# Optimization experiments

Hardware: AMD Instinct MI355X
Metric: run time of the kernel (lower is better)

Reference implementation:

```python
import jax, jax.numpy as jnp
import numpy as np

B, S, QW, HID, HEADS = 1, 4096, 512, 512, 8
D = HID // HEADS  # size_per_head = 64
SCALE = 1.0 / np.sqrt(float(D))


def setup_inputs() -> dict:
    key = jax.random.key(0)
    k1, k2, k3, k4, k5 = jax.random.split(key, 5)
    return {
        "tensor_q": jax.random.normal(k1, (B, S, QW), dtype=jnp.float32),
        "tensor_k": jax.random.normal(k2, (B, S, QW), dtype=jnp.float32),
        "tensor_v": jax.random.normal(k3, (B, S, QW), dtype=jnp.float32),
        # in_proj_layer: [3*hidden, q_width] (torch uses rand uniform init; randn fine for reference)
        "in_proj": jax.random.normal(k4, (3 * HID, QW), dtype=jnp.float32) * 0.02,
        # out_proj: nn.Linear(hidden, out, bias=False) weight shape [out, hidden]
        "w_out": jax.random.normal(k5, (HID, HID), dtype=jnp.float32) * 0.02,
    }


def reference(tensor_q, tensor_k, tensor_v, in_proj, w_out):
    b, s, _ = tensor_q.shape
    wq, wk, wv = in_proj[:HID], in_proj[HID:2 * HID], in_proj[2 * HID:]
    # mm(W, x_2d^T)^T  ==  x_2d @ W^T ; reshape to [b, s, heads, d]
    q = (tensor_q.reshape(-1, QW) @ wq.T).reshape(b, s, HEADS, D)
    k = (tensor_k.reshape(-1, QW) @ wk.T).reshape(b, s, HEADS, D)
    v = (tensor_v.reshape(-1, QW) @ wv.T).reshape(b, s, HEADS, D)
    # scores: [b, h, s_q, s_k], explicitly materialized as in the source
    scores = jnp.einsum('bqhd,bkhd->bhqk', q, k) * SCALE
    probs = jax.nn.softmax(scores, axis=-1)
    ctx = jnp.einsum('bhqk,bkhd->bqhd', probs, v).reshape(b * s, HID)
    out = ctx @ w_out.T
    return out.reshape(b, s, HID)
```

## Files before the change

### kernel.cpp

```cpp
#include <hip/hip_runtime.h>
#include <hip/hip_bf16.h>

#define S_LEN 4096
#define QW_K  512
#define HID_N 512
#define HEADS 8
#define DH    64
#define QSCALE (0.125f * 1.4426950408889634f)

typedef _Float16 f16;
typedef _Float16 half8  __attribute__((ext_vector_type(8)));
typedef _Float16 half4v __attribute__((ext_vector_type(4)));
typedef float    float4v __attribute__((ext_vector_type(4)));
typedef float    f32x16 __attribute__((ext_vector_type(16)));
typedef unsigned int uint;
typedef unsigned int uint4v __attribute__((ext_vector_type(4)));

__device__ inline uint pkh(float a, float b) {
    return __builtin_bit_cast(uint, __builtin_amdgcn_cvt_pkrtz(a, b));
}
__device__ inline void plswap(uint& a, uint& b) {
    asm volatile("v_permlane32_swap_b32 %0, %1" : "+v"(a), "+v"(b));
}


__global__ __launch_bounds__(256) void proj_kernel(
    const float* __restrict__ xq, const float* __restrict__ xk,
    const float* __restrict__ xv, const float* __restrict__ in_proj,
    f16* __restrict__ qws, f16* __restrict__ kws, f16* __restrict__ vtws)
{
    __shared__ f16 As[128][40];
    __shared__ f16 Ws[128][40];

    const int tid  = threadIdx.x;
    const int lane = tid & 63;
    const int w    = tid >> 6;
    const int wm   = w >> 1, wn = w & 1;
    const int l15  = lane & 15, g = lane >> 4;
    const int m0   = blockIdx.x * 128;
    const int n0   = blockIdx.y * 128;
    const int matid = n0 >> 9;
    const float* A = (matid == 0) ? xq : (matid == 1) ? xk : xv;

    float4v acc[4][4];
    for (int i = 0; i < 4; i++)
        for (int j = 0; j < 4; j++)
            for (int r = 0; r < 4; r++) acc[i][j][r] = 0.0f;

    const int srow = tid >> 3;
    const int scol = (tid & 7) * 4;

    for (int k0 = 0; k0 < QW_K; k0 += 32) {
        __syncthreads();
        #pragma unroll
        for (int p = 0; p < 4; p++) {
            int r = p * 32 + srow;
            float4v av = *(const float4v*)(A + (size_t)(m0 + r) * QW_K + k0 + scol);
            float4v wv = *(const float4v*)(in_proj + (size_t)(n0 + r) * QW_K + k0 + scol);
            half4v ah, wh;
            for (int e = 0; e < 4; e++) { ah[e] = (f16)av[e]; wh[e] = (f16)wv[e]; }
            *(half4v*)&As[r][scol] = ah;
            *(half4v*)&Ws[r][scol] = wh;
        }
        __syncthreads();

        half8 a[4], b[4];
        #pragma unroll
        for (int i = 0; i < 4; i++) a[i] = *(const half8*)&As[wm * 64 + i * 16 + l15][g * 8];
        #pragma unroll
        for (int j = 0; j < 4; j++) b[j] = *(const half8*)&Ws[wn * 64 + j * 16 + l15][g * 8];
        #pragma unroll
        for (int i = 0; i < 4; i++)
            #pragma unroll
            for (int j = 0; j < 4; j++)
                acc[i][j] = __builtin_amdgcn_mfma_f32_16x16x32_f16(a[i], b[j], acc[i][j], 0, 0, 0);
    }

    #pragma unroll
    for (int i = 0; i < 4; i++) {
        int grow0 = m0 + wm * 64 + i * 16 + g * 4;
        #pragma unroll
        for (int j = 0; j < 4; j++) {
            int gcol = n0 + wn * 64 + j * 16 + l15;
            int c = gcol & 511;
            int h = c >> 6, d = c & 63;
            if (matid == 2) {
                int db = d >> 5, l31v = d & 31;
                int kb16 = grow0 >> 4;
                int g5v  = (grow0 >> 3) & 1;
                int e0   = grow0 & 7;
                half4v pv;
                for (int r = 0; r < 4; r++) pv[r] = (f16)acc[i][j][r];
                *(half4v*)(vtws + ((size_t)((h * 2 + db) * 256 + kb16) << 9)
                                + l31v * 16 + g5v * 8 + e0) = pv;
            } else if (matid == 0) {
                for (int r = 0; r < 4; r++)
                    qws[((size_t)h * S_LEN + grow0 + r) * DH + d] = (f16)(acc[i][j][r] * QSCALE);
            } else {
                int dblk = d >> 4, g5k = (d >> 3) & 1, e = d & 7;
                for (int r = 0; r < 4; r++) {
                    int s = grow0 + r;
                    kws[((size_t)((h * 128 + (s >> 5)) * 4 + dblk) << 9)
                        + (s & 31) * 16 + g5k * 8 + e] = (f16)acc[i][j][r];
                }
            }
        }
    }
}

__global__ __launch_bounds__(256) void attn_kernel(
    const f16* __restrict__ qws, const f16* __restrict__ kws,
    const f16* __restrict__ vtws, f16* __restrict__ ctxws)
{
    __shared__ float Ol[4][32][68];
    __shared__ float Ls[4][32];

    const int tid  = threadIdx.x;
    const int lane = tid & 63;
    const int w    = tid >> 6;
    const int l31  = lane & 31;
    const int g5   = lane >> 5;
    const int blk  = blockIdx.x;
    const int h    = blk & 7;
    const int qb   = blk >> 3;
    const int q0   = qb * 32;

    const f16* Kf = kws  + ((size_t)h * 128 * 4 << 9);
    const f16* Vf = vtws + ((size_t)h * 2 * 256 << 9);
    const int lo = l31 * 16 + g5 * 8;

    half8 qf[4];
    {
        const f16* qp = qws + ((size_t)h * S_LEN + q0 + l31) * DH + g5 * 8;
        #pragma unroll
        for (int dblk = 0; dblk < 4; dblk++)
            qf[dblk] = *(const half8*)(qp + dblk * 16);
    }

    float lsum = 0.0f;
    f32x16 oacc0, oacc1;
    #pragma unroll
    for (int i = 0; i < 16; i++) { oacc0[i] = 0.0f; oacc1[i] = 0.0f; }

    const int kt0 = w * 32;

    half8 kf[2][4];
    #pragma unroll
    for (int kb32 = 0; kb32 < 2; kb32++)
        #pragma unroll
        for (int dblk = 0; dblk < 4; dblk++)
            kf[kb32][dblk] = *(const half8*)(Kf + ((size_t)((kt0 + kb32) * 4 + dblk) << 9) + lo);

    for (int t = 0; t < 16; t++) {
        const int kv0 = (w * 16 + t) * 64;

        half8 vf[2][4];
        #pragma unroll
        for (int db = 0; db < 2; db++)
            #pragma unroll
            for (int kb = 0; kb < 4; kb++)
                vf[db][kb] = *(const half8*)(Vf
                    + ((size_t)((db << 8) + (kv0 >> 4) + kb) << 9) + lo);

        f32x16 st0, st1;
        #pragma unroll
        for (int i = 0; i < 16; i++) { st0[i] = 0.0f; st1[i] = 0.0f; }
        #pragma unroll
        for (int dblk = 0; dblk < 4; dblk++) {
            st0 = __builtin_amdgcn_mfma_f32_32x32x16_f16(kf[0][dblk], qf[dblk], st0, 0, 0, 0);
            st1 = __builtin_amdgcn_mfma_f32_32x32x16_f16(kf[1][dblk], qf[dblk], st1, 0, 0, 0);
        }

        {
            const int ktn = (t < 15) ? kt0 + t * 2 + 2 : kt0;
            #pragma unroll
            for (int kb32 = 0; kb32 < 2; kb32++)
                #pragma unroll
                for (int dblk = 0; dblk < 4; dblk++)
                    kf[kb32][dblk] = *(const half8*)(Kf
                        + ((size_t)((ktn + kb32) * 4 + dblk) << 9) + lo);
        }

        #pragma unroll
        for (int i = 0; i < 16; i++) {
            st0[i] = exp2f(st0[i]);
            st1[i] = exp2f(st1[i]);
        }

        f32x16 ss;
        #pragma unroll
        for (int i = 0; i < 16; i++) ss[i] = st0[i] + st1[i];
        #pragma unroll
        for (int off = 8; off >= 1; off >>= 1)
            #pragma unroll
            for (int i = 0; i < off; i++) ss[i] += ss[i + off];
        lsum += ss[0];

        half8 pf[4];
        #pragma unroll
        for (int kb = 0; kb < 2; kb++) {
            uint w0 = pkh(st0[8 * kb + 0], st0[8 * kb + 1]);
            uint w1 = pkh(st0[8 * kb + 2], st0[8 * kb + 3]);
            uint w2 = pkh(st0[8 * kb + 4], st0[8 * kb + 5]);
            uint w3 = pkh(st0[8 * kb + 6], st0[8 * kb + 7]);
            plswap(w0, w2);
            plswap(w1, w3);
            uint4v u; u[0] = w0; u[1] = w1; u[2] = w2; u[3] = w3;
            pf[kb] = __builtin_bit_cast(half8, u);
        }
        #pragma unroll
        for (int kb = 0; kb < 2; kb++) {
            uint w0 = pkh(st1[8 * kb + 0], st1[8 * kb + 1]);
            uint w1 = pkh(st1[8 * kb + 2], st1[8 * kb + 3]);
            uint w2 = pkh(st1[8 * kb + 4], st1[8 * kb + 5]);
            uint w3 = pkh(st1[8 * kb + 6], st1[8 * kb + 7]);
            plswap(w0, w2);
            plswap(w1, w3);
            uint4v u; u[0] = w0; u[1] = w1; u[2] = w2; u[3] = w3;
            pf[2 + kb] = __builtin_bit_cast(half8, u);
        }

        #pragma unroll
        for (int kb = 0; kb < 4; kb++) {
            oacc0 = __builtin_amdgcn_mfma_f32_32x32x16_f16(vf[0][kb], pf[kb], oacc0, 0, 0, 0);
            oacc1 = __builtin_amdgcn_mfma_f32_32x32x16_f16(vf[1][kb], pf[kb], oacc1, 0, 0, 0);
        }
    }

    lsum += __shfl_xor(lsum, 32);
    #pragma unroll
    for (int rg = 0; rg < 4; rg++) {
        float4v v0, v1;
        #pragma unroll
        for (int j = 0; j < 4; j++) { v0[j] = oacc0[rg * 4 + j]; v1[j] = oacc1[rg * 4 + j]; }
        const int dd = rg * 8 + g5 * 4;
        *(float4v*)&Ol[w][l31][dd]      = v0;
        *(float4v*)&Ol[w][l31][32 + dd] = v1;
    }
    if (g5 == 0) Ls[w][l31] = lsum;
    __syncthreads();

    #pragma unroll
    for (int it = 0; it < 2; it++) {
        int qd = tid * 2 + it;
        int q  = qd >> 4;
        int dd = (qd & 15) * 4;
        float4v s0 = *(const float4v*)&Ol[0][q][dd];
        float4v s1 = *(const float4v*)&Ol[1][q][dd];
        float4v s2 = *(const float4v*)&Ol[2][q][dd];
        float4v s3 = *(const float4v*)&Ol[3][q][dd];
        float inv = 1.0f / (Ls[0][q] + Ls[1][q] + Ls[2][q] + Ls[3][q]);
        half4v o;
        #pragma unroll
        for (int j = 0; j < 4; j++)
            o[j] = (f16)((s0[j] + s1[j] + s2[j] + s3[j]) * inv);
        *(half4v*)(ctxws + (size_t)(q0 + q) * HID_N + h * DH + dd) = o;
    }
}

__global__ __launch_bounds__(256) void outproj_kernel(
    const f16* __restrict__ ctxws, const float* __restrict__ w_out,
    float* __restrict__ out)
{
    __shared__ f16 As[128][40];
    __shared__ f16 Ws[128][40];

    const int tid  = threadIdx.x;
    const int lane = tid & 63;
    const int w    = tid >> 6;
    const int wm   = w >> 1, wn = w & 1;
    const int l15  = lane & 15, g = lane >> 4;
    const int m0   = blockIdx.x * 128;
    const int n0   = blockIdx.y * 128;

    float4v acc[4][4];
    for (int i = 0; i < 4; i++)
        for (int j = 0; j < 4; j++)
            for (int r = 0; r < 4; r++) acc[i][j][r] = 0.0f;

    const int arow = tid >> 2;
    const int acg  = (tid & 3) * 8;
    const int srow = tid >> 3;
    const int scol = (tid & 7) * 4;

    for (int k0 = 0; k0 < HID_N; k0 += 32) {
        __syncthreads();
        #pragma unroll
        for (int p = 0; p < 2; p++) {
            int r = p * 64 + arow;
            *(half8*)&As[r][acg] =
                *(const half8*)(ctxws + (size_t)(m0 + r) * HID_N + k0 + acg);
        }
        #pragma unroll
        for (int p = 0; p < 4; p++) {
            int r = p * 32 + srow;
            float4v wv = *(const float4v*)(w_out + (size_t)(n0 + r) * HID_N + k0 + scol);
            half4v wh;
            for (int e = 0; e < 4; e++) wh[e] = (f16)wv[e];
            *(half4v*)&Ws[r][scol] = wh;
        }
        __syncthreads();

        half8 a[4], b[4];
        #pragma unroll
        for (int i = 0; i < 4; i++) a[i] = *(const half8*)&As[wm * 64 + i * 16 + l15][g * 8];
        #pragma unroll
        for (int j = 0; j < 4; j++) b[j] = *(const half8*)&Ws[wn * 64 + j * 16 + l15][g * 8];
        #pragma unroll
        for (int i = 0; i < 4; i++)
            #pragma unroll
            for (int j = 0; j < 4; j++)
                acc[i][j] = __builtin_amdgcn_mfma_f32_16x16x32_f16(a[i], b[j], acc[i][j], 0, 0, 0);
    }

    #pragma unroll
    for (int i = 0; i < 4; i++) {
        int grow0 = m0 + wm * 64 + i * 16 + g * 4;
        #pragma unroll
        for (int j = 0; j < 4; j++) {
            int gcol = n0 + wn * 64 + j * 16 + l15;
            for (int r = 0; r < 4; r++)
                out[(size_t)(grow0 + r) * HID_N + gcol] = acc[i][j][r];
        }
    }
}

extern "C" void kernel_launch(void* const* d_in, const int* in_sizes, int n_in,
                              void* d_out, int out_size, void* d_ws, size_t ws_size,
                              hipStream_t stream)
{
    const float* xq      = (const float*)d_in[0];
    const float* xk      = (const float*)d_in[1];
    const float* xv      = (const float*)d_in[2];
    const float* in_proj = (const float*)d_in[3];
    const float* w_out   = (const float*)d_in[4];
    float* out = (float*)d_out;

    const size_t per = (size_t)HEADS * S_LEN * DH;
    f16* qws   = (f16*)d_ws;
    f16* kws   = qws + per;
    f16* vtws  = kws + per;
    f16* ctxws = vtws + per;

    proj_kernel<<<dim3(32, 12), 256, 0, stream>>>(xq, xk, xv, in_proj, qws, kws, vtws);
    attn_kernel<<<dim3(1024), 256, 0, stream>>>(qws, kws, vtws, ctxws);
    outproj_kernel<<<dim3(32, 4), 256, 0, stream>>>(ctxws, w_out, out);
}
```

Before: 103.1 us.

## Tree-reduce attention partials, raw v_exp, MFMA priority, fp32 context output

Replaces the exp2f calls with a raw v_exp_f32 inline asm and raises wave priority around the MFMA blocks using s_setprio. The cross-wave reduction of partial outputs becomes a two-level tree through a smaller LDS buffer. Wave 0 then normalizes and writes the context directly from registers as fp32, instead of all threads summing four partials and writing fp16. The out-projection now reads the fp32 context and converts it to fp16 while staging. This doubles context traffic and adds extra barriers in exchange for less LDS use and a simpler epilogue.

Measured after the change: 100.8 us. 2.2% less time.

```diff
diff --git a/kernel.cpp b/kernel.cpp
--- a/kernel.cpp
+++ b/kernel.cpp
@@ -21,6 +21,11 @@
 }
 __device__ inline void plswap(uint& a, uint& b) {
     asm volatile("v_permlane32_swap_b32 %0, %1" : "+v"(a), "+v"(b));
+}
+__device__ inline float hexp2(float x) {
+    float r;
+    asm("v_exp_f32 %0, %1" : "=v"(r) : "v"(x));
+    return r;
 }
 
 
@@ -110,10 +115,10 @@
 
 __global__ __launch_bounds__(256) void attn_kernel(
     const f16* __restrict__ qws, const f16* __restrict__ kws,
-    const f16* __restrict__ vtws, f16* __restrict__ ctxws)
+    const f16* __restrict__ vtws, float* __restrict__ ctxws)
 {
-    __shared__ float Ol[4][32][68];
-    __shared__ float Ls[4][32];
+    __shared__ float Ol[2][32][68];
+    __shared__ float Ls[2][32];
 
     const int tid  = threadIdx.x;
     const int lane = tid & 63;
@@ -165,11 +170,13 @@
         f32x16 st0, st1;
         #pragma unroll
         for (int i = 0; i < 16; i++) { st0[i] = 0.0f; st1[i] = 0.0f; }
+        __builtin_amdgcn_s_setprio(1);
         #pragma unroll
         for (int dblk = 0; dblk < 4; dblk++) {
             st0 = __builtin_amdgcn_mfma_f32_32x32x16_f16(kf[0][dblk], qf[dblk], st0, 0, 0, 0);
             st1 = __builtin_amdgcn_mfma_f32_32x32x16_f16(kf[1][dblk], qf[dblk], st1, 0, 0, 0);
         }
+        __builtin_amdgcn_s_setprio(0);
 
         {
             const int ktn = (t < 15) ? kt0 + t * 2 + 2 : kt0;
@@ -183,8 +190,8 @@
 
         #pragma unroll
         for (int i = 0; i < 16; i++) {
-            st0[i] = exp2f(st0[i]);
-            st1[i] = exp2f(st1[i]);
+            st0[i] = hexp2(st0[i]);
+            st1[i] = hexp2(st1[i]);
         }
 
         f32x16 ss;
@@ -220,46 +227,85 @@
             pf[2 + kb] = __builtin_bit_cast(half8, u);
         }
 
+        __builtin_amdgcn_s_setprio(1);
         #pragma unroll
         for (int kb = 0; kb < 4; kb++) {
             oacc0 = __builtin_amdgcn_mfma_f32_32x32x16_f16(vf[0][kb], pf[kb], oacc0, 0, 0, 0);
             oacc1 = __builtin_amdgcn_mfma_f32_32x32x16_f16(vf[1][kb], pf[kb], oacc1, 0, 0, 0);
         }
+        __builtin_amdgcn_s_setprio(0);
     }
 
     lsum += __shfl_xor(lsum, 32);
-    #pragma unroll
-    for (int rg = 0; rg < 4; rg++) {
-        float4v v0, v1;
-        #pragma unroll
-        for (int j = 0; j < 4; j++) { v0[j] = oacc0[rg * 4 + j]; v1[j] = oacc1[rg * 4 + j]; }
-        const int dd = rg * 8 + g5 * 4;
-        *(float4v*)&Ol[w][l31][dd]      = v0;
-        *(float4v*)&Ol[w][l31][32 + dd] = v1;
-    }
-    if (g5 == 0) Ls[w][l31] = lsum;
+
+    if (w & 1) {
+        #pragma unroll
+        for (int rg = 0; rg < 4; rg++) {
+            float4v v0, v1;
+            #pragma unroll
+            for (int j = 0; j < 4; j++) { v0[j] = oacc0[rg * 4 + j]; v1[j] = oacc1[rg * 4 + j]; }
+            const int dd = rg * 8 + g5 * 4;
+            *(float4v*)&Ol[w >> 1][l31][dd]      = v0;
+            *(float4v*)&Ol[w >> 1][l31][32 + dd] = v1;
+        }
+        if (g5 == 0) Ls[w >> 1][l31] = lsum;
+    }
     __syncthreads();
-
-    #pragma unroll
-    for (int it = 0; it < 2; it++) {
-        int qd = tid * 2 + it;
-        int q  = qd >> 4;
-        int dd = (qd & 15) * 4;
-        float4v s0 = *(const float4v*)&Ol[0][q][dd];
-        float4v s1 = *(const float4v*)&Ol[1][q][dd];
-        float4v s2 = *(const float4v*)&Ol[2][q][dd];
-        float4v s3 = *(const float4v*)&Ol[3][q][dd];
-        float inv = 1.0f / (Ls[0][q] + Ls[1][q] + Ls[2][q] + Ls[3][q]);
-        half4v o;
-        #pragma unroll
-        for (int j = 0; j < 4; j++)
-            o[j] = (f16)((s0[j] + s1[j] + s2[j] + s3[j]) * inv);
-        *(half4v*)(ctxws + (size_t)(q0 + q) * HID_N + h * DH + dd) = o;
+    if (!(w & 1)) {
+        const int buf = w >> 1;
+        #pragma unroll
+        for (int rg = 0; rg < 4; rg++) {
+            const int dd = rg * 8 + g5 * 4;
+            float4v v0 = *(const float4v*)&Ol[buf][l31][dd];
+            float4v v1 = *(const float4v*)&Ol[buf][l31][32 + dd];
+            #pragma unroll
+            for (int j = 0; j < 4; j++) { oacc0[rg * 4 + j] += v0[j]; oacc1[rg * 4 + j] += v1[j]; }
+        }
+        lsum += Ls[buf][l31];
+    }
+    __syncthreads();
+    if (w == 2) {
+        #pragma unroll
+        for (int rg = 0; rg < 4; rg++) {
+            float4v v0, v1;
+            #pragma unroll
+            for (int j = 0; j < 4; j++) { v0[j] = oacc0[rg * 4 + j]; v1[j] = oacc1[rg * 4 + j]; }
+            const int dd = rg * 8 + g5 * 4;
+            *(float4v*)&Ol[1][l31][dd]      = v0;
+            *(float4v*)&Ol[1][l31][32 + dd] = v1;
+        }
+        if (g5 == 0) Ls[1][l31] = lsum;
+    }
+    __syncthreads();
+    if (w == 0) {
+        #pragma unroll
+        for (int rg = 0; rg < 4; rg++) {
+            const int dd = rg * 8 + g5 * 4;
+            float4v v0 = *(const float4v*)&Ol[1][l31][dd];
+            float4v v1 = *(const float4v*)&Ol[1][l31][32 + dd];
+            #pragma unroll
+            for (int j = 0; j < 4; j++) { oacc0[rg * 4 + j] += v0[j]; oacc1[rg * 4 + j] += v1[j]; }
+        }
+        lsum += Ls[1][l31];
+        const float inv = 1.0f / lsum;
+        float* cbase = ctxws + (size_t)(q0 + l31) * HID_N + h * DH;
+        #pragma unroll
+        for (int rg = 0; rg < 4; rg++) {
+            float4v v0, v1;
+            #pragma unroll
+            for (int j = 0; j < 4; j++) {
+                v0[j] = oacc0[rg * 4 + j] * inv;
+                v1[j] = oacc1[rg * 4 + j] * inv;
+            }
+            const int dd = rg * 8 + g5 * 4;
+            *(float4v*)(cbase + dd)      = v0;
+            *(float4v*)(cbase + 32 + dd) = v1;
+        }
     }
 }
 
 __global__ __launch_bounds__(256) void outproj_kernel(
-    const f16* __restrict__ ctxws, const float* __restrict__ w_out,
+    const float* __restrict__ ctxws, const float* __restrict__ w_out,
     float* __restrict__ out)
 {
     __shared__ f16 As[128][40];
@@ -278,25 +324,19 @@
         for (int j = 0; j < 4; j++)
             for (int r = 0; r < 4; r++) acc[i][j][r] = 0.0f;
 
-    const int arow = tid >> 2;
-    const int acg  = (tid & 3) * 8;
     const int srow = tid >> 3;
     const int scol = (tid & 7) * 4;
 
     for (int k0 = 0; k0 < HID_N; k0 += 32) {
         __syncthreads();
         #pragma unroll
-        for (int p = 0; p < 2; p++) {
-            int r = p * 64 + arow;
-            *(half8*)&As[r][acg] =
-                *(const half8*)(ctxws + (size_t)(m0 + r) * HID_N + k0 + acg);
-        }
-        #pragma unroll
         for (int p = 0; p < 4; p++) {
             int r = p * 32 + srow;
+            float4v av = *(const float4v*)(ctxws + (size_t)(m0 + r) * HID_N + k0 + scol);
             float4v wv = *(const float4v*)(w_out + (size_t)(n0 + r) * HID_N + k0 + scol);
-            half4v wh;
-            for (int e = 0; e < 4; e++) wh[e] = (f16)wv[e];
+            half4v ah, wh;
+            for (int e = 0; e < 4; e++) { ah[e] = (f16)av[e]; wh[e] = (f16)wv[e]; }
+            *(half4v*)&As[r][scol] = ah;
             *(half4v*)&Ws[r][scol] = wh;
         }
         __syncthreads();
@@ -340,7 +380,7 @@
     f16* qws   = (f16*)d_ws;
     f16* kws   = qws + per;
     f16* vtws  = kws + per;
-    f16* ctxws = vtws + per;
+    float* ctxws = (float*)(vtws + per);
 
     proj_kernel<<<dim3(32, 12), 256, 0, stream>>>(xq, xk, xv, in_proj, qws, kws, vtws);
     attn_kernel<<<dim3(1024), 256, 0, stream>>>(qws, kws, vtws, ctxws);
```
